# Performance work log

Measured on AMD Instinct MI355X. Metric: run time of the kernel, lower is better.

The kernel has to match this reference:

```python
import jax, jax.numpy as jnp
import numpy as np

B, S, D, H = 2, 2048, 1024, 16
HD = D // H

def setup_inputs() -> dict:
    key = jax.random.key(0)
    ks = jax.random.split(key, 5)
    sc = 1.0 / np.sqrt(D)
    return {
        "x": jax.random.normal(ks[0], (B, S, D), dtype=jnp.float32),
        "Wq": jax.random.normal(ks[1], (D, D), dtype=jnp.float32) * sc,
        "bq": jnp.zeros((D,), jnp.float32),
        "Wk": jax.random.normal(ks[2], (D, D), dtype=jnp.float32) * sc,
        "bk": jnp.zeros((D,), jnp.float32),
        "Wv": jax.random.normal(ks[3], (D, D), dtype=jnp.float32) * sc,
        "bv": jnp.zeros((D,), jnp.float32),
        "Wo": jax.random.normal(ks[4], (D, D), dtype=jnp.float32) * sc,
        "bo": jnp.zeros((D,), jnp.float32),
    }

def reference(x, Wq, bq, Wk, bk, Wv, bv, Wo, bo):
    b, s, d = x.shape
    def proj(W, bias):
        # [B,S,D] -> [B,H,S,HD]
        return (x @ W + bias).reshape(b, s, H, HD).swapaxes(1, 2)
    q = proj(Wq, bq)
    k = proj(Wk, bk)
    v = proj(Wv, bv)
    # naive full attention, matching the module (materializes [B,H,S,S])
    logits = jnp.einsum("bhqd,bhkd->bhqk", q, k) / jnp.sqrt(jnp.float32(HD))
    attn = jax.nn.softmax(logits, axis=-1)
    vals = jnp.einsum("bhqk,bhkd->bhqd", attn, v)
    vals = vals.swapaxes(1, 2).reshape(b, s, d)
    return vals @ Wo + bo
```

## Files before the change

kernel.cpp:

```cpp
#include <hip/hip_runtime.h>

typedef unsigned short u16;
typedef __bf16 bf16x8 __attribute__((ext_vector_type(8)));
typedef __bf16 bf16x4 __attribute__((ext_vector_type(4)));
typedef float f32x4 __attribute__((ext_vector_type(4)));

__device__ __forceinline__ u16 f2bf(float f) {
    union { float f; unsigned int i; } v;
    v.f = f;
    unsigned int u = v.i;
    return (u16)((u + 0x7fffu + ((u >> 16) & 1u)) >> 16);
}

__device__ __forceinline__ void dma16(const void* g, void* l) {
    __builtin_amdgcn_global_load_lds(
        (__attribute__((address_space(1))) void*)g,
        (__attribute__((address_space(3))) void*)l, 16, 0, 0);
}


__global__ __launch_bounds__(256) void cvt_w4(
    const float* __restrict__ W0, const float* __restrict__ W1,
    const float* __restrict__ W2, const float* __restrict__ W3,
    u16* __restrict__ out) {
    __shared__ u16 t[32][33];
    int z = blockIdx.z;
    const float* in = (z == 0) ? W0 : (z == 1) ? W1 : (z == 2) ? W2 : W3;
    u16* o = out + (size_t)z * 1048576;
    int bx = blockIdx.x * 32, by = blockIdx.y * 32;
    int tx = threadIdx.x & 31, ty = threadIdx.x >> 5;
#pragma unroll
    for (int i = 0; i < 32; i += 8)
        t[ty + i][tx] = f2bf(in[(size_t)(by + ty + i) * 1024 + bx + tx]);
    __syncthreads();
#pragma unroll
    for (int i = 0; i < 32; i += 8) {
        int n = bx + ty + i, k = by + tx;
        o[(size_t)n * 1024 + (k ^ ((n & 7) << 3))] = t[tx][ty + i];
    }
}

__global__ __launch_bounds__(256) void cvt_x(const float* __restrict__ in,
                                             u16* __restrict__ out) {
    int i = blockIdx.x * 256 + threadIdx.x;
    int s = i >> 8, k = (i & 255) * 4;
    float4 f = reinterpret_cast<const float4*>(in)[i];
    ushort4 h;
    h.x = f2bf(f.x); h.y = f2bf(f.y); h.z = f2bf(f.z); h.w = f2bf(f.w);
    *reinterpret_cast<ushort4*>(&out[(size_t)s * 1024 + (k ^ ((s & 7) << 3))]) = h;
}

__global__ __launch_bounds__(256) void gemm_qkv(
    const u16* __restrict__ xbf, const u16* __restrict__ wt,
    const float* __restrict__ bq, const float* __restrict__ bk,
    const float* __restrict__ bv,
    u16* __restrict__ qkg, u16* __restrict__ vgt) {
    __shared__ __align__(16) u16 As[128 * 64];
    __shared__ __align__(16) u16 Bs[128 * 64];

    int tid = threadIdx.x;
    int m0 = blockIdx.y * 128, n0 = blockIdx.x * 128;
    int wave = tid >> 6, lane = tid & 63;
    int wm = (wave >> 1) * 64, wn = (wave & 1) * 64;
    int l16 = lane & 15, quad = lane >> 4;
    int sl = l16 & 7;

    int seg = n0 >> 10;
    int n0r = n0 & 1023;
    const u16* WT = wt + (size_t)seg * 1048576;
    bool swp = (seg == 2);

    f32x4 acc[4][4];
#pragma unroll
    for (int mi = 0; mi < 4; mi++)
#pragma unroll
        for (int ni = 0; ni < 4; ni++) acc[mi][ni] = (f32x4){0.f, 0.f, 0.f, 0.f};

    int rsub = lane >> 3, c16 = (lane & 7) * 8;
    for (int k0 = 0; k0 < 1024; k0 += 64) {
#pragma unroll
        for (int i = 0; i < 4; i++) {
            int row = wave * 32 + i * 8 + rsub;
            dma16(&xbf[(size_t)(m0 + row) * 1024 + k0 + c16], &As[wave * 2048 + i * 512]);
            dma16(&WT[(size_t)(n0r + row) * 1024 + k0 + c16], &Bs[wave * 2048 + i * 512]);
        }
        __syncthreads();
        const u16* Am = swp ? Bs : As;
        const u16* Bn = swp ? As : Bs;
#pragma unroll
        for (int kk = 0; kk < 64; kk += 32) {
            int co = ((((kk >> 3) + quad) ^ sl) << 3);
            bf16x8 af[4], bf[4];
#pragma unroll
            for (int mi = 0; mi < 4; mi++)
                af[mi] = *reinterpret_cast<const bf16x8*>(
                    &Am[(wm + mi * 16 + l16) * 64 + co]);
#pragma unroll
            for (int ni = 0; ni < 4; ni++)
                bf[ni] = *reinterpret_cast<const bf16x8*>(
                    &Bn[(wn + ni * 16 + l16) * 64 + co]);
#pragma unroll
            for (int mi = 0; mi < 4; mi++)
#pragma unroll
                for (int ni = 0; ni < 4; ni++)
                    acc[mi][ni] = __builtin_amdgcn_mfma_f32_16x16x32_bf16(
                        af[mi], bf[ni], acc[mi][ni], 0, 0, 0);
        }
        __syncthreads();
    }

    if (!swp) {
#pragma unroll
        for (int ni = 0; ni < 4; ni++) {
            int n = n0 + wn + ni * 16 + l16;
            float bb = (n < 1024) ? bq[n] : bk[n - 1024];
#pragma unroll
            for (int mi = 0; mi < 4; mi++)
#pragma unroll
                for (int r = 0; r < 4; r++) {
                    int s = m0 + wm + mi * 16 + quad * 4 + r;
                    int key = (seg == 0) ? (s & 7) : ((s >> 2) & 7);
                    int col = n ^ (key << 3);
                    qkg[(size_t)(s >> 11) * 4194304 + (size_t)(s & 2047) * 2048 + col] =
                        f2bf(acc[mi][ni][r] + bb);
                }
        }
    } else {
#pragma unroll
        for (int mi = 0; mi < 4; mi++)
#pragma unroll
            for (int r = 0; r < 4; r++) {
                int v = n0r + wm + mi * 16 + quad * 4 + r;
                float bb = bv[v];
#pragma unroll
                for (int ni = 0; ni < 4; ni++) {
                    int s = m0 + wn + ni * 16 + l16;
                    int scol = (s & 2047) ^ ((v & 7) << 3);
                    vgt[(size_t)((s >> 11) * 1024 + v) * 2048 + scol] =
                        f2bf(acc[mi][ni][r] + bb);
                }
            }
    }
}

#define SC2 0.18033688f

__global__ __launch_bounds__(256) void attention_kern(
    u16* __restrict__ qkg, const u16* __restrict__ vgt) {
    __shared__ __align__(16) u16 Ks[2][64 * 64];
    __shared__ __align__(16) u16 Vt[2][64 * 64];
    __shared__ __align__(16) u16 Ps[64 * 64];

    int tid = threadIdx.x;
    int qt = blockIdx.x, h = blockIdx.y, b = blockIdx.z;
    int wave = tid >> 6, lane = tid & 63;
    int l16 = lane & 15, quad = lane >> 4;
    int rsub = lane >> 3, c16 = (lane & 7) * 8;
    int sl = l16 & 7;

    u16* qb = qkg + (size_t)b * 4194304 + (size_t)(qt * 64) * 2048 + h * 64;
    const u16* kb = qkg + (size_t)b * 4194304 + 1024 + h * 64;
    const u16* vb = vgt + (size_t)(b * 1024 + h * 64) * 2048;

    bf16x8 qf[2];
    {
        const u16* qr = qb + (size_t)(wave * 16 + l16) * 2048;
        qf[0] = *reinterpret_cast<const bf16x8*>(&qr[(quad ^ sl) << 3]);
        qf[1] = *reinterpret_cast<const bf16x8*>(&qr[((4 + quad) ^ sl) << 3]);
    }

    float lp[4];
    f32x4 o[4];
#pragma unroll
    for (int r = 0; r < 4; r++) lp[r] = 0.f;
#pragma unroll
    for (int ni = 0; ni < 4; ni++) o[ni] = (f32x4){0.f, 0.f, 0.f, 0.f};

    auto STAGE = [&](int kt, int bi) {
        const u16* ktb = kb + (size_t)(kt * 64) * 2048;
        const u16* vtb = vb + kt * 64;
#pragma unroll
        for (int i = 0; i < 2; i++) {
            int gk = 32 * i + 4 * rsub + wave;
            dma16(&ktb[(size_t)gk * 2048 + c16], &Ks[bi][wave * 1024 + i * 512]);
            int rv = wave * 16 + i * 8 + rsub;
            dma16(&vtb[(size_t)rv * 2048 + c16], &Vt[bi][wave * 1024 + i * 512]);
        }
    };

    STAGE(0, 0);

    for (int kt = 0; kt < 32; kt++) {
        int cur = kt & 1;
        if (kt < 31) {
            STAGE(kt + 1, cur ^ 1);
            asm volatile("s_waitcnt vmcnt(4)\n\ts_barrier" ::: "memory");
        } else {
            asm volatile("s_waitcnt vmcnt(0)\n\ts_barrier" ::: "memory");
        }

        f32x4 s[4];
#pragma unroll
        for (int ni = 0; ni < 4; ni++) s[ni] = (f32x4){0.f, 0.f, 0.f, 0.f};
#pragma unroll
        for (int kk = 0; kk < 64; kk += 32) {
            int co = ((((kk >> 3) + quad) ^ sl) << 3);
            bf16x8 af = qf[kk >> 5];
#pragma unroll
            for (int ni = 0; ni < 4; ni++) {
                bf16x8 bfr = *reinterpret_cast<const bf16x8*>(
                    &Ks[cur][(ni * 16 + l16) * 64 + co]);
                s[ni] = __builtin_amdgcn_mfma_f32_16x16x32_bf16(af, bfr, s[ni], 0, 0, 0);
            }
        }

#pragma unroll
        for (int r = 0; r < 4; r++) {
            float p0 = __builtin_amdgcn_exp2f(s[0][r] * SC2);
            float p1 = __builtin_amdgcn_exp2f(s[1][r] * SC2);
            float p2 = __builtin_amdgcn_exp2f(s[2][r] * SC2);
            float p3 = __builtin_amdgcn_exp2f(s[3][r] * SC2);
            lp[r] += (p0 + p1) + (p2 + p3);
            f32x4 pf = {p0, p1, p2, p3};
            bf16x4 pb = __builtin_convertvector(pf, bf16x4);
            int q = wave * 16 + quad * 4 + r;
            *reinterpret_cast<bf16x4*>(
                &Ps[q * 64 + (((l16 >> 1) ^ (q & 7)) << 3) + (l16 & 1) * 4]) = pb;
        }

#pragma unroll
        for (int kk = 0; kk < 64; kk += 32) {
            int co = ((((kk >> 3) + quad) ^ sl) << 3);
            bf16x8 af = *reinterpret_cast<const bf16x8*>(
                &Ps[(wave * 16 + l16) * 64 + co]);
#pragma unroll
            for (int ni = 0; ni < 4; ni++) {
                bf16x8 bfr = *reinterpret_cast<const bf16x8*>(
                    &Vt[cur][(ni * 16 + l16) * 64 + co]);
                o[ni] = __builtin_amdgcn_mfma_f32_16x16x32_bf16(af, bfr, o[ni], 0, 0, 0);
            }
        }
        asm volatile("s_waitcnt lgkmcnt(0)\n\ts_barrier" ::: "memory");
    }

    float inv[4];
#pragma unroll
    for (int r = 0; r < 4; r++) {
        float v = lp[r];
#pragma unroll
        for (int off = 1; off < 16; off <<= 1) v += __shfl_xor(v, off);
        inv[r] = __builtin_amdgcn_rcpf(v);
    }
#pragma unroll
    for (int ni = 0; ni < 4; ni++)
#pragma unroll
        for (int r = 0; r < 4; r++) {
            int s = qt * 64 + wave * 16 + quad * 4 + r;
            int d = h * 64 + ni * 16 + l16;
            qkg[(size_t)b * 4194304 + (size_t)s * 2048 + (d ^ ((s & 7) << 3))] =
                f2bf(o[ni][r] * inv[r]);
        }
}

__global__ __launch_bounds__(256) void gemm_out(
    const u16* __restrict__ attb, const u16* __restrict__ wot,
    const float* __restrict__ bo, float* __restrict__ out) {
    __shared__ __align__(16) u16 As[128 * 64];
    __shared__ __align__(16) u16 Bs[64 * 64];

    int tid = threadIdx.x;
    int m0 = blockIdx.y * 128, n0 = blockIdx.x * 64;
    int wave = tid >> 6, lane = tid & 63;
    int wm = (wave >> 1) * 64, wn = (wave & 1) * 32;
    int l16 = lane & 15, quad = lane >> 4;
    int sl = l16 & 7;
    int rsub = lane >> 3, c16 = (lane & 7) * 8;

    f32x4 acc[4][2];
#pragma unroll
    for (int mi = 0; mi < 4; mi++)
#pragma unroll
        for (int ni = 0; ni < 2; ni++) acc[mi][ni] = (f32x4){0.f, 0.f, 0.f, 0.f};

    for (int k0 = 0; k0 < 1024; k0 += 64) {
#pragma unroll
        for (int i = 0; i < 4; i++) {
            int row = wave * 32 + i * 8 + rsub;
            dma16(&attb[(size_t)(m0 + row) * 2048 + k0 + c16], &As[wave * 2048 + i * 512]);
        }
#pragma unroll
        for (int i = 0; i < 2; i++) {
            int row = wave * 16 + i * 8 + rsub;
            dma16(&wot[(size_t)(n0 + row) * 1024 + k0 + c16], &Bs[wave * 1024 + i * 512]);
        }
        __syncthreads();
#pragma unroll
        for (int kk = 0; kk < 64; kk += 32) {
            int co = ((((kk >> 3) + quad) ^ sl) << 3);
            bf16x8 af[4], bf[2];
#pragma unroll
            for (int mi = 0; mi < 4; mi++)
                af[mi] = *reinterpret_cast<const bf16x8*>(
                    &As[(wm + mi * 16 + l16) * 64 + co]);
#pragma unroll
            for (int ni = 0; ni < 2; ni++)
                bf[ni] = *reinterpret_cast<const bf16x8*>(
                    &Bs[(wn + ni * 16 + l16) * 64 + co]);
#pragma unroll
            for (int mi = 0; mi < 4; mi++)
#pragma unroll
                for (int ni = 0; ni < 2; ni++)
                    acc[mi][ni] = __builtin_amdgcn_mfma_f32_16x16x32_bf16(
                        af[mi], bf[ni], acc[mi][ni], 0, 0, 0);
        }
        __syncthreads();
    }

#pragma unroll
    for (int ni = 0; ni < 2; ni++) {
        int n = n0 + wn + ni * 16 + l16;
        float bb = bo[n];
#pragma unroll
        for (int mi = 0; mi < 4; mi++)
#pragma unroll
            for (int r = 0; r < 4; r++)
                out[(size_t)(m0 + wm + mi * 16 + quad * 4 + r) * 1024 + n] =
                    acc[mi][ni][r] + bb;
    }
}

extern "C" void kernel_launch(void* const* d_in, const int* in_sizes, int n_in,
                              void* d_out, int out_size, void* d_ws, size_t ws_size,
                              hipStream_t stream) {
    const float* x  = (const float*)d_in[0];
    const float* Wq = (const float*)d_in[1];
    const float* bq = (const float*)d_in[2];
    const float* Wk = (const float*)d_in[3];
    const float* bk = (const float*)d_in[4];
    const float* Wv = (const float*)d_in[5];
    const float* bv = (const float*)d_in[6];
    const float* Wo = (const float*)d_in[7];
    const float* bo = (const float*)d_in[8];

    u16* WT  = (u16*)d_out;
    u16* xbf = (u16*)d_out + 4 * 1048576;
    u16* QKg = (u16*)d_ws;
    u16* Vgt = (u16*)d_ws + 8 * 1048576;

    cvt_w4<<<dim3(32, 32, 4), 256, 0, stream>>>(Wq, Wk, Wv, Wo, WT);
    cvt_x<<<4096, 256, 0, stream>>>(x, xbf);

    gemm_qkv<<<dim3(24, 32), 256, 0, stream>>>(xbf, WT, bq, bk, bv, QKg, Vgt);

    attention_kern<<<dim3(32, 16, 2), 256, 0, stream>>>(QKg, Vgt);

    hipMemcpyAsync(Vgt, WT + 3 * 1048576, (size_t)2 * 1048576,
                   hipMemcpyDeviceToDevice, stream);
    gemm_out<<<dim3(16, 32), 256, 0, stream>>>(QKg, Vgt, bo, (float*)d_out);
}
```

Before: 216.9 us.

## Enlarge attention query tile, fold softmax scale into Q, compute row sums via MFMA

The attention kernel now uses 512 threads, so each block handles 128 query rows and every staged K/V tile is shared by twice as many queries. Each thread issues one DMA per tile instead of two, and the wait count is adjusted to match. The softmax scale is applied to Q in the QKV GEMM epilogue, which removes a multiply per score. Row sums come from an MFMA against a vector of ones rather than scalar adds plus shuffles. The launch grid is flattened and remapped, likely to group blocks that share a head, and the sums are now taken over bf16-rounded probabilities, which changes precision slightly.

```diff
diff --git a/kernel.cpp b/kernel.cpp
--- a/kernel.cpp
+++ b/kernel.cpp
@@ -4,6 +4,8 @@
 typedef __bf16 bf16x8 __attribute__((ext_vector_type(8)));
 typedef __bf16 bf16x4 __attribute__((ext_vector_type(4)));
 typedef float f32x4 __attribute__((ext_vector_type(4)));
+
+#define SC2 0.18033688f
 
 __device__ __forceinline__ u16 f2bf(float f) {
     union { float f; unsigned int i; } v;
@@ -110,6 +112,7 @@
     }
 
     if (!swp) {
+        float sc = (seg == 0) ? SC2 : 1.0f;
 #pragma unroll
         for (int ni = 0; ni < 4; ni++) {
             int n = n0 + wn + ni * 16 + l16;
@@ -122,7 +125,7 @@
                     int key = (seg == 0) ? (s & 7) : ((s >> 2) & 7);
                     int col = n ^ (key << 3);
                     qkg[(size_t)(s >> 11) * 4194304 + (size_t)(s & 2047) * 2048 + col] =
-                        f2bf(acc[mi][ni][r] + bb);
+                        f2bf((acc[mi][ni][r] + bb) * sc);
                 }
         }
     } else {
@@ -143,22 +146,23 @@
     }
 }
 
-#define SC2 0.18033688f
-
-__global__ __launch_bounds__(256) void attention_kern(
+__global__ __launch_bounds__(512) void attention_kern(
     u16* __restrict__ qkg, const u16* __restrict__ vgt) {
     __shared__ __align__(16) u16 Ks[2][64 * 64];
     __shared__ __align__(16) u16 Vt[2][64 * 64];
-    __shared__ __align__(16) u16 Ps[64 * 64];
+    __shared__ __align__(16) u16 Ps[128 * 64];
 
     int tid = threadIdx.x;
-    int qt = blockIdx.x, h = blockIdx.y, b = blockIdx.z;
+    int bid = blockIdx.x;
+    int id = (bid & 7) * 64 + (bid >> 3);
+    int qt = id & 15, h = (id >> 4) & 15, b = id >> 8;
+
     int wave = tid >> 6, lane = tid & 63;
     int l16 = lane & 15, quad = lane >> 4;
     int rsub = lane >> 3, c16 = (lane & 7) * 8;
     int sl = l16 & 7;
 
-    u16* qb = qkg + (size_t)b * 4194304 + (size_t)(qt * 64) * 2048 + h * 64;
+    u16* qb = qkg + (size_t)b * 4194304 + (size_t)(qt * 128) * 2048 + h * 64;
     const u16* kb = qkg + (size_t)b * 4194304 + 1024 + h * 64;
     const u16* vb = vgt + (size_t)(b * 1024 + h * 64) * 2048;
 
@@ -169,23 +173,23 @@
         qf[1] = *reinterpret_cast<const bf16x8*>(&qr[((4 + quad) ^ sl) << 3]);
     }
 
-    float lp[4];
-    f32x4 o[4];
-#pragma unroll
-    for (int r = 0; r < 4; r++) lp[r] = 0.f;
+    bf16x8 onef;
+#pragma unroll
+    for (int i = 0; i < 8; i++) onef[i] = (__bf16)1.0f;
+
+    f32x4 o[4], ls;
 #pragma unroll
     for (int ni = 0; ni < 4; ni++) o[ni] = (f32x4){0.f, 0.f, 0.f, 0.f};
+    ls = (f32x4){0.f, 0.f, 0.f, 0.f};
+
+    int r8 = wave * 8 + rsub;
+    int gk = 4 * (r8 & 15) + (r8 >> 4);
 
     auto STAGE = [&](int kt, int bi) {
         const u16* ktb = kb + (size_t)(kt * 64) * 2048;
         const u16* vtb = vb + kt * 64;
-#pragma unroll
-        for (int i = 0; i < 2; i++) {
-            int gk = 32 * i + 4 * rsub + wave;
-            dma16(&ktb[(size_t)gk * 2048 + c16], &Ks[bi][wave * 1024 + i * 512]);
-            int rv = wave * 16 + i * 8 + rsub;
-            dma16(&vtb[(size_t)rv * 2048 + c16], &Vt[bi][wave * 1024 + i * 512]);
-        }
+        dma16(&ktb[(size_t)gk * 2048 + c16], &Ks[bi][wave * 512]);
+        dma16(&vtb[(size_t)r8 * 2048 + c16], &Vt[bi][wave * 512]);
     };
 
     STAGE(0, 0);
@@ -194,7 +198,7 @@
         int cur = kt & 1;
         if (kt < 31) {
             STAGE(kt + 1, cur ^ 1);
-            asm volatile("s_waitcnt vmcnt(4)\n\ts_barrier" ::: "memory");
+            asm volatile("s_waitcnt vmcnt(2)\n\ts_barrier" ::: "memory");
         } else {
             asm volatile("s_waitcnt vmcnt(0)\n\ts_barrier" ::: "memory");
         }
@@ -216,12 +220,10 @@
 
 #pragma unroll
         for (int r = 0; r < 4; r++) {
-            float p0 = __builtin_amdgcn_exp2f(s[0][r] * SC2);
-            float p1 = __builtin_amdgcn_exp2f(s[1][r] * SC2);
-            float p2 = __builtin_amdgcn_exp2f(s[2][r] * SC2);
-            float p3 = __builtin_amdgcn_exp2f(s[3][r] * SC2);
-            lp[r] += (p0 + p1) + (p2 + p3);
-            f32x4 pf = {p0, p1, p2, p3};
+            f32x4 pf = {__builtin_amdgcn_exp2f(s[0][r]),
+                        __builtin_amdgcn_exp2f(s[1][r]),
+                        __builtin_amdgcn_exp2f(s[2][r]),
+                        __builtin_amdgcn_exp2f(s[3][r])};
             bf16x4 pb = __builtin_convertvector(pf, bf16x4);
             int q = wave * 16 + quad * 4 + r;
             *reinterpret_cast<bf16x4*>(
@@ -233,6 +235,7 @@
             int co = ((((kk >> 3) + quad) ^ sl) << 3);
             bf16x8 af = *reinterpret_cast<const bf16x8*>(
                 &Ps[(wave * 16 + l16) * 64 + co]);
+            ls = __builtin_amdgcn_mfma_f32_16x16x32_bf16(af, onef, ls, 0, 0, 0);
 #pragma unroll
             for (int ni = 0; ni < 4; ni++) {
                 bf16x8 bfr = *reinterpret_cast<const bf16x8*>(
@@ -245,17 +248,12 @@
 
     float inv[4];
 #pragma unroll
-    for (int r = 0; r < 4; r++) {
-        float v = lp[r];
-#pragma unroll
-        for (int off = 1; off < 16; off <<= 1) v += __shfl_xor(v, off);
-        inv[r] = __builtin_amdgcn_rcpf(v);
-    }
+    for (int r = 0; r < 4; r++) inv[r] = __builtin_amdgcn_rcpf(ls[r]);
 #pragma unroll
     for (int ni = 0; ni < 4; ni++)
 #pragma unroll
         for (int r = 0; r < 4; r++) {
-            int s = qt * 64 + wave * 16 + quad * 4 + r;
+            int s = qt * 128 + wave * 16 + quad * 4 + r;
             int d = h * 64 + ni * 16 + l16;
             qkg[(size_t)b * 4194304 + (size_t)s * 2048 + (d ^ ((s & 7) << 3))] =
                 f2bf(o[ni][r] * inv[r]);
@@ -352,7 +350,7 @@
 
     gemm_qkv<<<dim3(24, 32), 256, 0, stream>>>(xbf, WT, bq, bk, bv, QKg, Vgt);
 
-    attention_kern<<<dim3(32, 16, 2), 256, 0, stream>>>(QKg, Vgt);
+    attention_kern<<<dim3(512), 512, 0, stream>>>(QKg, Vgt);
 
     hipMemcpyAsync(Vgt, WT + 3 * 1048576, (size_t)2 * 1048576,
                    hipMemcpyDeviceToDevice, stream);
```

Measured after the change: 197.0 us. 9.2% less time.
